# Optimization experiments

Measured on AMD Instinct MI355X. Metric: run time of the kernel, lower is better.

Reference implementation:

```python
import jax, jax.numpy as jnp
import numpy as np

B, T, K = 256, 512, 128          # batch, seq_len, n_tag
START, STOP = 126, 127           # tag2idx[START_TAG], tag2idx[STOP_TAG]
NEG = -10000.0                   # same constant the torch module uses


def setup_inputs() -> dict:
    key = jax.random.key(0)
    k1, k2, k3 = jax.random.split(key, 3)
    feats = jax.random.normal(k1, (B, T, K), dtype=jnp.float32)
    tags = jax.random.randint(k2, (B, T), 0, 126)  # never START/STOP
    # learned CRF transition matrix: trans[to, from]
    transitions = 0.1 * jax.random.normal(k3, (K, K), dtype=jnp.float32)
    transitions = transitions.at[START, :].set(NEG).at[:, STOP].set(NEG)
    return {"feats": feats, "tags": tags, "transitions": transitions}


def _forward_alg(feats, trans):
    """Batched CRF forward algorithm. feats [B,T,K] -> log Z [B]."""
    b = feats.shape[0]
    init = jnp.full((b, K), NEG, feats.dtype).at[:, START].set(0.0)

    def step(alpha, feat_t):
        # scores[b, to, from] = alpha[b, from] + trans[to, from]
        scores = alpha[:, None, :] + trans[None, :, :]
        alpha_new = jax.nn.logsumexp(scores, axis=-1) + feat_t
        return alpha_new, None

    alpha, _ = jax.lax.scan(step, init, jnp.swapaxes(feats, 0, 1))
    return jax.nn.logsumexp(alpha + trans[STOP][None, :], axis=-1)


def _score_sentence(feats, tags, trans):
    """Batched gold path score. feats [B,T,K], tags [B,T] -> [B]."""
    b = feats.shape[0]
    start_col = jnp.full((b, 1), START, tags.dtype)
    tags_ext = jnp.concatenate([start_col, tags], axis=1)      # [B,T+1]
    trans_sc = trans[tags_ext[:, 1:], tags_ext[:, :-1]].sum(axis=1)
    emit_sc = jnp.take_along_axis(feats, tags[..., None], axis=2)[..., 0].sum(axis=1)
    return trans_sc + emit_sc + trans[STOP, tags[:, -1]]


def _viterbi(feats, trans):
    """Batched Viterbi decode. Returns (path_score [B], path [B,T])."""
    b = feats.shape[0]
    init = jnp.full((b, K), NEG, feats.dtype).at[:, START].set(0.0)

    def step(alpha, feat_t):
        scores = alpha[:, None, :] + trans[None, :, :]   # [B,to,from]
        bptr = jnp.argmax(scores, axis=-1)               # [B,to]
        alpha_new = jnp.max(scores, axis=-1) + feat_t
        return alpha_new, bptr

    alpha, bptrs = jax.lax.scan(step, init, jnp.swapaxes(feats, 0, 1))
    term = alpha + trans[STOP][None, :]
    last_tag = jnp.argmax(term, axis=-1)                 # [B]
    path_score = jnp.max(term, axis=-1)

    def back(tag_t, bp_t):
        prev = jnp.take_along_axis(bp_t, tag_t[:, None], axis=1)[:, 0]
        return prev, tag_t

    _, path = jax.lax.scan(back, last_tag, bptrs, reverse=True)  # [T,B]
    return path_score, jnp.swapaxes(path, 0, 1)


def reference(feats, tags, transitions):
    log_z = _forward_alg(feats, transitions)             # forward_alg per sentence
    gold = _score_sentence(feats, tags, transitions)     # score_sentence
    path_score, pred = _viterbi(feats, transitions)      # viterbi_decode
    loss = jnp.sum(log_z - gold) / jnp.float32(feats.shape[0] * feats.shape[1])
    return loss, path_score, pred
```

## Files before the change

kernel.cpp:

```cpp
#include <hip/hip_runtime.h>
#include <cstdint>
#include <cstddef>

#define BB 256
#define TT 512
#define KK 128
#define START_TAG 126
#define STOP_TAG 127
#define NEGV (-10000.0f)
#define NINF (-__builtin_huge_valf())

template<int CTRL>
__device__ __forceinline__ float dppf(float v, float old) {
  return __int_as_float(__builtin_amdgcn_update_dpp(
      __float_as_int(old), __float_as_int(v), CTRL, 0xf, 0xf, false));
}
template<int CTRL>
__device__ __forceinline__ int dppi(int v, int old) {
  return __builtin_amdgcn_update_dpp(old, v, CTRL, 0xf, 0xf, false);
}
__device__ __forceinline__ float wave_max63(float x) {
  x = fmaxf(x, dppf<0x111>(x, NINF));
  x = fmaxf(x, dppf<0x112>(x, NINF));
  x = fmaxf(x, dppf<0x114>(x, NINF));
  x = fmaxf(x, dppf<0x118>(x, NINF));
  x = fmaxf(x, dppf<0x142>(x, NINF));
  x = fmaxf(x, dppf<0x143>(x, NINF));
  return x;
}
__device__ __forceinline__ float max3f(float a, float b, float c) {
  float d;
  asm("v_max3_f32 %0, %1, %2, %3" : "=v"(d) : "v"(a), "v"(b), "v"(c));
  return d;
}
__device__ __forceinline__ int paddr(int i) { return (i >> 5) * 36 + (i & 31); }

__global__ __launch_bounds__(1024, 4) void crf1024(
    const float* __restrict__ feats, const float* __restrict__ trans,
    const int* __restrict__ tags,
    float* __restrict__ pscore, int* __restrict__ lasttag,
    float* __restrict__ alphaS, float* __restrict__ gb)
{
  const int b = blockIdx.x;
  const int tid = threadIdx.x;
  const bool isv = tid < 512;
  const int q = isv ? tid : tid - 512;
  const int to = q >> 2;
  const int h  = q & 3;
  const int lane = tid & 63;
  const int wv = tid >> 6;

  __shared__ __align__(16) float AV[2][144];
  __shared__ __align__(16) float P [2][144];
  __shared__ __align__(16) float pwm[8];
  __shared__ float vitm[2]; __shared__ int viti[2];
  __shared__ float reds[2]; __shared__ float redg[8];

  float R[32];
  {
    const float4* tr = (const float4*)(trans + (size_t)to * KK + h * 32);
#pragma unroll
    for (int c = 0; c < 8; ++c) {
      float4 v = tr[c];
      if (isv) { R[4*c+0]=v.x; R[4*c+1]=v.y; R[4*c+2]=v.z; R[4*c+3]=v.w; }
      else     { R[4*c+0]=__expf(v.x); R[4*c+1]=__expf(v.y);
                 R[4*c+2]=__expf(v.z); R[4*c+3]=__expf(v.w); }
    }
  }
#pragma unroll
  for (int c = 0; c < 32; ++c) asm volatile("" : "+v"(R[c]));

  if (isv) { if (h == 0) AV[0][paddr(to)] = (to==START_TAG)?0.0f:NEGV; }
  else     { if (h == 0) P[0][paddr(to)]  = (to==START_TAG)?1.0f:0.0f; }
  __syncthreads();

  const float* fb = feats + (size_t)b * TT * KK + to;
  float* aSb = alphaS + (size_t)b * TT * KK + to;

  float M = 0.0f;
  float fcur = fb[0];
  int cur = 0;

#pragma unroll 4
  for (int t = 0; t < TT; ++t) {
    const int tn = (t + 1 < TT) ? t + 1 : t;
    float fnext = fb[(size_t)tn * KK];

    if (isv) {
      const float* Ac = &AV[cur][0];
      const int base = h * 36;
      float4 p = *(const float4*)&Ac[base];
      float m0 = fmaxf(p.x + R[0], p.y + R[1]);
      float m1 = fmaxf(p.z + R[2], p.w + R[3]);
#pragma unroll
      for (int c = 1; c < 8; ++c) {
        p = *(const float4*)&Ac[base + c * 4];
        m0 = max3f(m0, p.x + R[4*c+0], p.y + R[4*c+1]);
        m1 = max3f(m1, p.z + R[4*c+2], p.w + R[4*c+3]);
      }
      float m = fmaxf(m0, m1);
      m = fmaxf(m, dppf<0xB1>(m, m));
      m = fmaxf(m, dppf<0x4E>(m, m));
      if (h == 0) {
        float a = m + fcur;
        AV[cur ^ 1][paddr(to)] = a;
        __builtin_nontemporal_store(a, &aSb[(size_t)t * KK]);
      }
    } else {
      float corr = 1.0f;
      if ((t & 3) == 0 && t) {
        float4 w0 = *(const float4*)&pwm[0];
        float4 w1 = *(const float4*)&pwm[4];
        float pmax = fmaxf(fmaxf(fmaxf(w0.x, w0.y), fmaxf(w0.z, w0.w)),
                           fmaxf(fmaxf(w1.x, w1.y), fmaxf(w1.z, w1.w)));
        M += __logf(pmax);
        corr = 1.0f / pmax;
      }
      const float* Pc = &P[cur][0];
      const int base = h * 36;
      float s0=0.f, s1=0.f, s2=0.f, s3=0.f;
#pragma unroll
      for (int c = 0; c < 8; ++c) {
        float4 p = *(const float4*)&Pc[base + c * 4];
        s0 = fmaf(R[4*c+0], p.x, s0);
        s1 = fmaf(R[4*c+1], p.y, s1);
        s2 = fmaf(R[4*c+2], p.z, s2);
        s3 = fmaf(R[4*c+3], p.w, s3);
      }
      float s = (s0 + s1) + (s2 + s3);
      s = s + dppf<0xB1>(s, s);
      s = s + dppf<0x4E>(s, s);
      float ef = __expf(fcur);
      if ((t & 3) == 0 && t) ef *= corr;
      float pv = s * ef;
      if (h == 0) P[cur ^ 1][paddr(to)] = pv;
      if ((t & 3) == 3) {
        float wm = wave_max63(pv);
        if (lane == 63) pwm[wv - 8] = wm;
      }
    }
    __syncthreads();
    cur ^= 1;
    fcur = fnext;
  }

  if (tid < KK) {
    float term = AV[cur][paddr(tid)] + trans[(size_t)STOP_TAG * KK + tid];
    float m = term; int i = tid;
#pragma unroll
    for (int off = 1; off < 64; off <<= 1) {
      float mo = __shfl_xor(m, off, 64);
      int   io = __shfl_xor(i, off, 64);
      if (mo > m || (mo == m && io < i)) { m = mo; i = io; }
    }
    if (lane == 0) { vitm[tid >> 6] = m; viti[tid >> 6] = i; }
  }
  if (tid >= 512 && tid < 512 + KK) {
    const int to2 = tid - 512;
    float e = P[cur][paddr(to2)] * __expf(trans[(size_t)STOP_TAG * KK + to2]);
#pragma unroll
    for (int off = 1; off < 64; off <<= 1) e += __shfl_xor(e, off, 64);
    if (lane == 0) reds[to2 >> 6] = e;
  }
  if (!isv) {
    const int* tg = tags + (size_t)b * TT;
    const float* fg = feats + (size_t)b * TT * KK;
    int ct = tg[q];
    int pv2 = (q == 0) ? START_TAG : tg[q - 1];
    float g = trans[(size_t)ct * KK + pv2] + fg[(size_t)q * KK + ct];
    if (q == TT - 1) g += trans[(size_t)STOP_TAG * KK + ct];
#pragma unroll
    for (int off = 1; off < 64; off <<= 1) g += __shfl_xor(g, off, 64);
    if (lane == 0) redg[wv - 8] = g;
  }
  __syncthreads();
  if (tid == 0) {
    float m = vitm[0]; int i = viti[0];
    if (vitm[1] > m || (vitm[1] == m && viti[1] < i)) { m = vitm[1]; i = viti[1]; }
    pscore[b] = m; lasttag[b] = i;
  }
  if (tid == 512) {
    float sg = redg[0]+redg[1]+redg[2]+redg[3]+redg[4]+redg[5]+redg[6]+redg[7];
    gb[b] = (M + __logf(reds[0] + reds[1])) - sg;
  }
}

__global__ __launch_bounds__(64) void backtrace_loss(
    const float* __restrict__ alphaS, const float* __restrict__ trans,
    const int* __restrict__ lasttag, const float* __restrict__ gb,
    float* __restrict__ pred, float* __restrict__ loss_out)
{
  const int lane = threadIdx.x;
  if (blockIdx.x == BB) {
    float v = gb[lane] + gb[lane + 64] + gb[lane + 128] + gb[lane + 192];
#pragma unroll
    for (int off = 1; off < 64; off <<= 1) v += __shfl_xor(v, off, 64);
    if (lane == 0) loss_out[0] = v / (float)(BB * TT);
    return;
  }
  const int b = blockIdx.x;
  __shared__ float tl[KK * KK];
  {
    const float4* src = (const float4*)trans;
    float4* dst = (float4*)tl;
#pragma unroll
    for (int i = 0; i < (KK * KK / 4) / 64; ++i) dst[lane + i * 64] = src[lane + i * 64];
  }
  int tag = lasttag[b];
  if (lane == 0) pred[(size_t)b * TT + (TT - 1)] = (float)tag;
  const float* arow = alphaS + (size_t)b * TT * KK;

  float p0[8], p1[8];
#pragma unroll
  for (int j = 0; j < 8; ++j) {
    int r = TT - 2 - j;
    p0[j] = arow[(size_t)r * KK + lane];
    p1[j] = arow[(size_t)r * KK + 64 + lane];
  }
  __syncthreads();

  for (int rb = TT - 2; rb >= 0; rb -= 8) {
#pragma unroll
    for (int j = 0; j < 8; ++j) {
      int r = rb - j;
      if (r >= 0) {
        float x0 = p0[j] + tl[tag * KK + lane];
        float x1 = p1[j] + tl[tag * KK + 64 + lane];
        float m = fmaxf(x0, x1);
        float M = wave_max63(m);
        M = __int_as_float(__builtin_amdgcn_readlane(__float_as_int(M), 63));
        unsigned long long b0 = __ballot(x0 == M);
        unsigned long long b1 = __ballot(x1 == M);
        tag = b0 ? (int)__builtin_ctzll(b0) : 64 + (int)__builtin_ctzll(b1);
        if (lane == 0) pred[(size_t)b * TT + r] = (float)tag;
        int rp = r - 8;
        if (rp >= 0) {
          p0[j] = arow[(size_t)rp * KK + lane];
          p1[j] = arow[(size_t)rp * KK + 64 + lane];
        }
      }
    }
  }
}

__global__ __launch_bounds__(768) void crf_main_fb(
    const float* __restrict__ feats, const float* __restrict__ trans,
    float* __restrict__ logz, float* __restrict__ pscore,
    int* __restrict__ lasttag, uint8_t* __restrict__ bptr)
{
  const int b = blockIdx.x;
  const int tid = threadIdx.x;
  const bool is_fwd = tid < 256;
  const int lane = tid & 63;

  __shared__ __align__(16) float P[2][144];
  __shared__ __align__(16) float AV[2][144];
  __shared__ __align__(16) float redmF[2][4];
  __shared__ float reds[4];
  __shared__ float vitm[8];
  __shared__ int   viti[8];

  int myto, h;
  if (is_fwd) { myto = tid >> 1; h = tid & 1; }
  else { int q = tid - 256; myto = q >> 2; h = q & 3; }

  float R[64];
  if (is_fwd) {
    const float4* tr = (const float4*)(trans + (size_t)myto * KK + h * 64);
#pragma unroll
    for (int c = 0; c < 16; ++c) {
      float4 v = tr[c];
      R[4*c+0]=expf(v.x); R[4*c+1]=expf(v.y); R[4*c+2]=expf(v.z); R[4*c+3]=expf(v.w);
    }
  } else {
    const float4* tr = (const float4*)(trans + (size_t)myto * KK + h * 32);
#pragma unroll
    for (int c = 0; c < 8; ++c) {
      float4 v = tr[c];
      R[4*c+0]=v.x; R[4*c+1]=v.y; R[4*c+2]=v.z; R[4*c+3]=v.w;
    }
  }

  if (is_fwd) { if (h == 0) P[0][paddr(myto)] = (myto==START_TAG)?1.0f:0.0f; }
  else        { if (h == 0) AV[0][paddr(myto)] = (myto==START_TAG)?0.0f:NEGV; }
  if (tid < 4) redmF[1][tid] = 0.0f;
  __syncthreads();

  const float* fb = feats + (size_t)b * TT * KK + myto;
  uint8_t* bp = bptr + (size_t)b * TT * KK + myto;

  float fcur = fb[0];
  float Mprev = 0.0f;
  float aCarry = 0.0f;
  int cur = 0;

  for (int t = 0; t < TT; ++t) {
    const int tn = (t + 1 < TT) ? t + 1 : t;
    float fnext = fb[(size_t)tn * KK];
    const int rd = (t + 1) & 1, wr = t & 1;

    if (is_fwd) {
      float4 rv = *(const float4*)&redmF[rd][0];
      float M1 = fmaxf(fmaxf(rv.x, rv.y), fmaxf(rv.z, rv.w));
      const float* Pc = &P[cur][0];
      const int base = h * 72;
      float s0=0.f, s1=0.f, s2=0.f, s3=0.f;
#pragma unroll
      for (int c = 0; c < 16; ++c) {
        float4 p = *(const float4*)&Pc[base + (c>>3)*36 + (c&7)*4];
        s0 = fmaf(R[4*c+0], p.x, s0);
        s1 = fmaf(R[4*c+1], p.y, s1);
        s2 = fmaf(R[4*c+2], p.z, s2);
        s3 = fmaf(R[4*c+3], p.w, s3);
      }
      float s = (s0 + s1) + (s2 + s3);
      s = s + dppf<0xB1>(s, s);
      float a = Mprev + logf(s) + fcur;
      float wm = wave_max63(a);
      if (lane == 63) redmF[wr][tid >> 6] = wm;
      float pv = expf(a - M1);
      if (h == 0) P[cur ^ 1][paddr(myto)] = pv;
      Mprev = M1;
      aCarry = a;
    } else {
      const float* Ac = &AV[cur][0];
      const int base = h * 36;
      const int fb0 = h * 32;
      float4 p0 = *(const float4*)&Ac[base];
      float m0 = p0.x + R[0], m1 = p0.y + R[1], m2 = p0.z + R[2], m3 = p0.w + R[3];
      int i0 = fb0, i1 = fb0+1, i2 = fb0+2, i3 = fb0+3;
#pragma unroll
      for (int c = 1; c < 8; ++c) {
        float4 p = *(const float4*)&Ac[base + c*4];
        float v0 = p.x + R[4*c+0]; if (v0 > m0) { m0 = v0; i0 = fb0+4*c+0; }
        float v1 = p.y + R[4*c+1]; if (v1 > m1) { m1 = v1; i1 = fb0+4*c+1; }
        float v2 = p.z + R[4*c+2]; if (v2 > m2) { m2 = v2; i2 = fb0+4*c+2; }
        float v3 = p.w + R[4*c+3]; if (v3 > m3) { m3 = v3; i3 = fb0+4*c+3; }
      }
      float m = m0; int i = i0;
      if (m1 > m || (m1 == m && i1 < i)) { m = m1; i = i1; }
      if (m2 > m || (m2 == m && i2 < i)) { m = m2; i = i2; }
      if (m3 > m || (m3 == m && i3 < i)) { m = m3; i = i3; }
      { float mo = dppf<0xB1>(m, m); int io = dppi<0xB1>(i, i);
        if (mo > m || (mo == m && io < i)) { m = mo; i = io; } }
      { float mo = dppf<0x4E>(m, m); int io = dppi<0x4E>(i, i);
        if (mo > m || (mo == m && io < i)) { m = mo; i = io; } }
      float a = m + fcur;
      if (h == 0) { AV[cur ^ 1][paddr(myto)] = a; bp[(size_t)t * KK] = (uint8_t)i; }
      aCarry = a;
    }
    __syncthreads();
    cur ^= 1;
    fcur = fnext;
  }

  float tstop = trans[(size_t)STOP_TAG * KK + myto];
  float term = aCarry + tstop;
  float M = 0.0f;
  if (is_fwd) {
    float wm = wave_max63(term);
    if (lane == 63) redmF[0][tid >> 6] = wm;
  } else {
    float m = term; int i = myto;
#pragma unroll
    for (int off = 1; off < 64; off <<= 1) {
      float mo = __shfl_xor(m, off, 64);
      int   io = __shfl_xor(i, off, 64);
      if (mo > m || (mo == m && io < i)) { m = mo; i = io; }
    }
    if (lane == 0) { vitm[(tid>>6)-4] = m; viti[(tid>>6)-4] = i; }
  }
  __syncthreads();
  if (is_fwd) {
    float4 rv = *(const float4*)&redmF[0][0];
    M = fmaxf(fmaxf(rv.x, rv.y), fmaxf(rv.z, rv.w));
    float e = (h == 0) ? expf(term - M) : 0.0f;
#pragma unroll
    for (int off = 1; off < 64; off <<= 1) e += __shfl_xor(e, off, 64);
    if (lane == 0) reds[tid >> 6] = e;
  } else if (tid == 256) {
    float m = vitm[0]; int i = viti[0];
#pragma unroll
    for (int w = 1; w < 8; ++w)
      if (vitm[w] > m || (vitm[w] == m && viti[w] < i)) { m = vitm[w]; i = viti[w]; }
    pscore[b] = m; lasttag[b] = i;
  }
  __syncthreads();
  if (tid == 0) logz[b] = M + logf(reds[0] + reds[1] + reds[2] + reds[3]);
}

__global__ __launch_bounds__(256) void backtrace_kernel(
    const uint8_t* __restrict__ bptr, const int* __restrict__ lasttag,
    float* __restrict__ pred)
{
  const int b = blockIdx.x;
  const int tid = threadIdx.x;
  __shared__ __align__(16) uint8_t lb[(TT / 2) * KK];
  __shared__ int tagcarry;
  if (tid == 0) tagcarry = lasttag[b];

  for (int half = 1; half >= 0; --half) {
    __syncthreads();
    const float4* src = reinterpret_cast<const float4*>(
        bptr + ((size_t)b * TT + (size_t)half * (TT / 2)) * KK);
    float4* dst = reinterpret_cast<float4*>(lb);
    for (int i = tid; i < (TT / 2) * KK / 16; i += 256) dst[i] = src[i];
    __syncthreads();
    if (tid == 0) {
      int tag = tagcarry;
      for (int t = TT / 2 - 1; t >= 0; --t) {
        int gt = half * (TT / 2) + t;
        pred[(size_t)b * TT + gt] = (float)tag;
        tag = lb[t * KK + tag];
      }
      tagcarry = tag;
    }
  }
}

__global__ __launch_bounds__(64) void gold_kernel(
    const float* __restrict__ feats, const int* __restrict__ tags,
    const float* __restrict__ trans, const float* __restrict__ logz,
    float* __restrict__ gb)
{
  const int b = blockIdx.x;
  const int lane = threadIdx.x;
  const int* tg = tags + (size_t)b * TT;
  const float* fb = feats + (size_t)b * TT * KK;
  float g = 0.0f;
#pragma unroll
  for (int k = 0; k < TT / 64; ++k) {
    int t = lane * (TT / 64) + k;
    int ct = tg[t];
    int pv = (t == 0) ? START_TAG : tg[t - 1];
    g += trans[ct * KK + pv] + fb[(size_t)t * KK + ct];
  }
  if (lane == 63) g += trans[STOP_TAG * KK + tg[TT - 1]];
#pragma unroll
  for (int off = 1; off <= 32; off <<= 1) g += __shfl_xor(g, off, 64);
  if (lane == 0) gb[b] = logz[b] - g;
}

__global__ __launch_bounds__(256) void loss_reduce(
    const float* __restrict__ gb, float* __restrict__ out)
{
  const int tid = threadIdx.x;
  const int lane = tid & 63, wv = tid >> 6;
  float v = gb[tid];
#pragma unroll
  for (int off = 1; off <= 32; off <<= 1) v += __shfl_xor(v, off, 64);
  __shared__ float red[4];
  if (lane == 0) red[wv] = v;
  __syncthreads();
  if (tid == 0) out[0] = (red[0] + red[1] + red[2] + red[3]) / (float)(BB * TT);
}

extern "C" void kernel_launch(void* const* d_in, const int* in_sizes, int n_in,
                              void* d_out, int out_size, void* d_ws, size_t ws_size,
                              hipStream_t stream) {
  const float* feats = (const float*)d_in[0];
  const int*   tags  = (const int*)d_in[1];
  const float* trans = (const float*)d_in[2];

  float* out    = (float*)d_out;
  float* loss   = out;
  float* pscore = out + 1;
  float* pred   = out + 1 + BB;
  (void)in_sizes; (void)n_in; (void)out_size;

  const size_t alpha_bytes = (size_t)BB * TT * KK * sizeof(float);
  const bool cheap = ws_size >= alpha_bytes + 4096;

  if (cheap) {
    float* alphaS  = (float*)d_ws;
    char*  wsend   = (char*)d_ws + alpha_bytes;
    int*   lasttag = (int*)(wsend);
    float* gb      = (float*)(wsend + BB * sizeof(int));
    crf1024<<<BB, 1024, 0, stream>>>(feats, trans, tags, pscore, lasttag,
                                     alphaS, gb);
    backtrace_loss<<<BB + 1, 64, 0, stream>>>(alphaS, trans, lasttag, gb,
                                              pred, loss);
  } else {
    uint8_t* bptr    = (uint8_t*)d_ws;
    char*    wsend   = (char*)d_ws + (size_t)BB * TT * KK;
    float*   logz    = (float*)(wsend);
    int*     lasttag = (int*)(wsend + BB * sizeof(float));
    float*   gb      = (float*)(wsend + BB * sizeof(float) + BB * sizeof(int));
    crf_main_fb<<<BB, 768, 0, stream>>>(feats, trans, logz, pscore, lasttag, bptr);
    backtrace_kernel<<<BB, 256, 0, stream>>>(bptr, lasttag, pred);
    gold_kernel<<<BB, 64, 0, stream>>>(feats, tags, trans, logz, gb);
    loss_reduce<<<1, 256, 0, stream>>>(gb, loss);
  }
}
```

Baseline: 379.0 us.

## Split Viterbi and forward recursions into separate 256-thread blocks

Each batch element's Viterbi and forward-algorithm recursions now run in two separate 256-thread blocks (512 blocks total) instead of one 1024-thread block. Each tag row is handled by 2 threads holding 64 transition values apiece, not 4 threads holding 32. This cuts the per-step barrier to 4 waves and removes one DPP reduction stage, at the cost of longer serial dot products per thread, more registers, and only one block per CU under the launch bound. The nontemporal alpha store also becomes a regular store.

Result: faster. 348.4 us, median of 2 (-8.1%).

```diff
diff --git a/kernel.cpp b/kernel.cpp
--- a/kernel.cpp
+++ b/kernel.cpp
@@ -35,43 +35,40 @@
 }
 __device__ __forceinline__ int paddr(int i) { return (i >> 5) * 36 + (i & 31); }
 
-__global__ __launch_bounds__(1024, 4) void crf1024(
+__global__ __launch_bounds__(256, 1) void crf256(
     const float* __restrict__ feats, const float* __restrict__ trans,
     const int* __restrict__ tags,
     float* __restrict__ pscore, int* __restrict__ lasttag,
     float* __restrict__ alphaS, float* __restrict__ gb)
 {
-  const int b = blockIdx.x;
+  const int bid = blockIdx.x;
+  const bool isv = bid < BB;
+  const int b = isv ? bid : bid - BB;
   const int tid = threadIdx.x;
-  const bool isv = tid < 512;
-  const int q = isv ? tid : tid - 512;
-  const int to = q >> 2;
-  const int h  = q & 3;
+  const int to = tid >> 1;
+  const int h  = tid & 1;
   const int lane = tid & 63;
   const int wv = tid >> 6;
 
-  __shared__ __align__(16) float AV[2][144];
-  __shared__ __align__(16) float P [2][144];
-  __shared__ __align__(16) float pwm[8];
+  __shared__ __align__(16) float BUF[2][144];
+  __shared__ __align__(16) float pwm[4];
   __shared__ float vitm[2]; __shared__ int viti[2];
-  __shared__ float reds[2]; __shared__ float redg[8];
-
-  float R[32];
+  __shared__ float reds[2]; __shared__ float redg[4];
+
+  float R[64];
   {
-    const float4* tr = (const float4*)(trans + (size_t)to * KK + h * 32);
-#pragma unroll
-    for (int c = 0; c < 8; ++c) {
+    const float4* tr = (const float4*)(trans + (size_t)to * KK + h * 64);
+#pragma unroll
+    for (int c = 0; c < 16; ++c) {
       float4 v = tr[c];
       if (isv) { R[4*c+0]=v.x; R[4*c+1]=v.y; R[4*c+2]=v.z; R[4*c+3]=v.w; }
       else     { R[4*c+0]=__expf(v.x); R[4*c+1]=__expf(v.y);
                  R[4*c+2]=__expf(v.z); R[4*c+3]=__expf(v.w); }
     }
   }
-#pragma unroll
-  for (int c = 0; c < 32; ++c) asm volatile("" : "+v"(R[c]));
-
-  if (isv) { if (h == 0) AV[0][paddr(to)] = (to==START_TAG)?0.0f:NEGV; }
-  else     { if (h == 0) P[0][paddr(to)]  = (to==START_TAG)?1.0f:0.0f; }
+
+  if (h == 0) BUF[0][paddr(to)] = isv ? ((to==START_TAG)?0.0f:NEGV)
+                                      : ((to==START_TAG)?1.0f:0.0f);
   __syncthreads();
 
   const float* fb = feats + (size_t)b * TT * KK + to;
@@ -85,43 +82,38 @@
   for (int t = 0; t < TT; ++t) {
     const int tn = (t + 1 < TT) ? t + 1 : t;
     float fnext = fb[(size_t)tn * KK];
+    const float* Bc = &BUF[cur][0];
+    const int base = h * 72;
 
     if (isv) {
-      const float* Ac = &AV[cur][0];
-      const int base = h * 36;
-      float4 p = *(const float4*)&Ac[base];
+      float4 p = *(const float4*)&Bc[base];
       float m0 = fmaxf(p.x + R[0], p.y + R[1]);
       float m1 = fmaxf(p.z + R[2], p.w + R[3]);
 #pragma unroll
-      for (int c = 1; c < 8; ++c) {
-        p = *(const float4*)&Ac[base + c * 4];
+      for (int c = 1; c < 16; ++c) {
+        p = *(const float4*)&Bc[base + (c>>3)*36 + (c&7)*4];
         m0 = max3f(m0, p.x + R[4*c+0], p.y + R[4*c+1]);
         m1 = max3f(m1, p.z + R[4*c+2], p.w + R[4*c+3]);
       }
       float m = fmaxf(m0, m1);
       m = fmaxf(m, dppf<0xB1>(m, m));
-      m = fmaxf(m, dppf<0x4E>(m, m));
       if (h == 0) {
         float a = m + fcur;
-        AV[cur ^ 1][paddr(to)] = a;
-        __builtin_nontemporal_store(a, &aSb[(size_t)t * KK]);
+        BUF[cur ^ 1][paddr(to)] = a;
+        aSb[(size_t)t * KK] = a;
       }
     } else {
       float corr = 1.0f;
       if ((t & 3) == 0 && t) {
-        float4 w0 = *(const float4*)&pwm[0];
-        float4 w1 = *(const float4*)&pwm[4];
-        float pmax = fmaxf(fmaxf(fmaxf(w0.x, w0.y), fmaxf(w0.z, w0.w)),
-                           fmaxf(fmaxf(w1.x, w1.y), fmaxf(w1.z, w1.w)));
+        float4 w = *(const float4*)&pwm[0];
+        float pmax = fmaxf(fmaxf(w.x, w.y), fmaxf(w.z, w.w));
         M += __logf(pmax);
         corr = 1.0f / pmax;
       }
-      const float* Pc = &P[cur][0];
-      const int base = h * 36;
       float s0=0.f, s1=0.f, s2=0.f, s3=0.f;
 #pragma unroll
-      for (int c = 0; c < 8; ++c) {
-        float4 p = *(const float4*)&Pc[base + c * 4];
+      for (int c = 0; c < 16; ++c) {
+        float4 p = *(const float4*)&Bc[base + (c>>3)*36 + (c&7)*4];
         s0 = fmaf(R[4*c+0], p.x, s0);
         s1 = fmaf(R[4*c+1], p.y, s1);
         s2 = fmaf(R[4*c+2], p.z, s2);
@@ -129,14 +121,13 @@
       }
       float s = (s0 + s1) + (s2 + s3);
       s = s + dppf<0xB1>(s, s);
-      s = s + dppf<0x4E>(s, s);
       float ef = __expf(fcur);
       if ((t & 3) == 0 && t) ef *= corr;
       float pv = s * ef;
-      if (h == 0) P[cur ^ 1][paddr(to)] = pv;
+      if (h == 0) BUF[cur ^ 1][paddr(to)] = pv;
       if ((t & 3) == 3) {
         float wm = wave_max63(pv);
-        if (lane == 63) pwm[wv - 8] = wm;
+        if (lane == 63) pwm[wv] = wm;
       }
     }
     __syncthreads();
@@ -144,44 +135,50 @@
     fcur = fnext;
   }
 
-  if (tid < KK) {
-    float term = AV[cur][paddr(tid)] + trans[(size_t)STOP_TAG * KK + tid];
-    float m = term; int i = tid;
-#pragma unroll
-    for (int off = 1; off < 64; off <<= 1) {
-      float mo = __shfl_xor(m, off, 64);
-      int   io = __shfl_xor(i, off, 64);
-      if (mo > m || (mo == m && io < i)) { m = mo; i = io; }
-    }
-    if (lane == 0) { vitm[tid >> 6] = m; viti[tid >> 6] = i; }
-  }
-  if (tid >= 512 && tid < 512 + KK) {
-    const int to2 = tid - 512;
-    float e = P[cur][paddr(to2)] * __expf(trans[(size_t)STOP_TAG * KK + to2]);
-#pragma unroll
-    for (int off = 1; off < 64; off <<= 1) e += __shfl_xor(e, off, 64);
-    if (lane == 0) reds[to2 >> 6] = e;
-  }
-  if (!isv) {
+  if (isv) {
+    if (tid < KK) {
+      float term = BUF[cur][paddr(tid)] + trans[(size_t)STOP_TAG * KK + tid];
+      float m = term; int i = tid;
+#pragma unroll
+      for (int off = 1; off < 64; off <<= 1) {
+        float mo = __shfl_xor(m, off, 64);
+        int   io = __shfl_xor(i, off, 64);
+        if (mo > m || (mo == m && io < i)) { m = mo; i = io; }
+      }
+      if (lane == 0) { vitm[tid >> 6] = m; viti[tid >> 6] = i; }
+    }
+    __syncthreads();
+    if (tid == 0) {
+      float m = vitm[0]; int i = viti[0];
+      if (vitm[1] > m || (vitm[1] == m && viti[1] < i)) { m = vitm[1]; i = viti[1]; }
+      pscore[b] = m; lasttag[b] = i;
+    }
+  } else {
+    if (tid < KK) {
+      float e = BUF[cur][paddr(tid)] * __expf(trans[(size_t)STOP_TAG * KK + tid]);
+#pragma unroll
+      for (int off = 1; off < 64; off <<= 1) e += __shfl_xor(e, off, 64);
+      if (lane == 0) reds[tid >> 6] = e;
+    }
     const int* tg = tags + (size_t)b * TT;
     const float* fg = feats + (size_t)b * TT * KK;
-    int ct = tg[q];
-    int pv2 = (q == 0) ? START_TAG : tg[q - 1];
-    float g = trans[(size_t)ct * KK + pv2] + fg[(size_t)q * KK + ct];
-    if (q == TT - 1) g += trans[(size_t)STOP_TAG * KK + ct];
+    float g = 0.0f;
+#pragma unroll
+    for (int k2 = 0; k2 < 2; ++k2) {
+      int t = tid + k2 * 256;
+      int ct = tg[t];
+      int pv2 = (t == 0) ? START_TAG : tg[t - 1];
+      g += trans[(size_t)ct * KK + pv2] + fg[(size_t)t * KK + ct];
+      if (t == TT - 1) g += trans[(size_t)STOP_TAG * KK + ct];
+    }
 #pragma unroll
     for (int off = 1; off < 64; off <<= 1) g += __shfl_xor(g, off, 64);
-    if (lane == 0) redg[wv - 8] = g;
-  }
-  __syncthreads();
-  if (tid == 0) {
-    float m = vitm[0]; int i = viti[0];
-    if (vitm[1] > m || (vitm[1] == m && viti[1] < i)) { m = vitm[1]; i = viti[1]; }
-    pscore[b] = m; lasttag[b] = i;
-  }
-  if (tid == 512) {
-    float sg = redg[0]+redg[1]+redg[2]+redg[3]+redg[4]+redg[5]+redg[6]+redg[7];
-    gb[b] = (M + __logf(reds[0] + reds[1])) - sg;
+    if (lane == 0) redg[wv] = g;
+    __syncthreads();
+    if (tid == 0) {
+      float sg = redg[0] + redg[1] + redg[2] + redg[3];
+      gb[b] = (M + __logf(reds[0] + reds[1])) - sg;
+    }
   }
 }
 
@@ -476,8 +473,8 @@
     char*  wsend   = (char*)d_ws + alpha_bytes;
     int*   lasttag = (int*)(wsend);
     float* gb      = (float*)(wsend + BB * sizeof(int));
-    crf1024<<<BB, 1024, 0, stream>>>(feats, trans, tags, pscore, lasttag,
-                                     alphaS, gb);
+    crf256<<<2 * BB, 256, 0, stream>>>(feats, trans, tags, pscore, lasttag,
+                                       alphaS, gb);
     backtrace_loss<<<BB + 1, 64, 0, stream>>>(alphaS, trans, lasttag, gb,
                                               pred, loss);
   } else {
```
